# Kernel optimization log

Hardware: AMD Instinct MI355X
Metric: run time of the kernel (lower is better)

## Reference

```python
import jax, jax.numpy as jnp
import numpy as np

EPS_LN = 1e-5
EPS_NORM = 1e-12


def _bilinear_matrix(in_size, out_size):
    # align_corners=True bilinear interpolation as a dense (out,in) matrix
    pos = np.arange(out_size) * (in_size - 1) / (out_size - 1)
    lo = np.floor(pos).astype(np.int64)
    hi = np.minimum(lo + 1, in_size - 1)
    frac = (pos - lo).astype(np.float32)
    M = np.zeros((out_size, in_size), np.float32)
    M[np.arange(out_size), lo] += 1.0 - frac
    M[np.arange(out_size), hi] += frac
    return jnp.asarray(M)

_M20 = _bilinear_matrix(7, 20)  # [20,7]


def _upsample(x):
    # bilinear 7x7 -> 20x20, align_corners=True: separable matmuls
    return jnp.einsum('ih,jw,nchw->ncij', _M20, _M20, x)


def _conv2d(x, w, b, stride, pad):
    out = jax.lax.conv_general_dilated(
        x, w, window_strides=(stride, stride),
        padding=[(pad, pad), (pad, pad)],
        dimension_numbers=('NCHW', 'OIHW', 'NCHW'))
    return out + b[None, :, None, None]


def _crn(x, t, ln_w, ln_b, w_t, b_t, w_s, b_s, w_m, b_m, w_l, b_l, acc_w, acc_b):
    # LayerNorm over last two dims [7,7] with elementwise affine
    mu = x.mean(axis=(-2, -1), keepdims=True)
    var = x.var(axis=(-2, -1), keepdims=True)
    xn = (x - mu) * jax.lax.rsqrt(var + EPS_LN) * ln_w + ln_b
    up = _upsample(xn)                      # [N,512,20,20]
    xs = _conv2d(up, w_s, b_s, 3, 1)        # [N,32,7,7]
    xm = _conv2d(up, w_m, b_m, 5, 9)        # [N,32,7,7]
    xl = _conv2d(up, w_l, b_l, 2, 1)        # [N,20,7,7]
    tu = _upsample(t)
    tc = _conv2d(tu, w_t, b_t, 2, 0)        # [N,16,7,7]
    cat = jnp.concatenate([xs, xm, xl, tc], axis=1)  # [N,100,7,7]
    return _conv2d(cat, acc_w, acc_b, 1, 0)          # [N,1,7,7]


def setup_inputs() -> dict:
    key = jax.random.key(0)
    ks = jax.random.split(key, 16)
    N, C, K = 512, 512, 64
    centroids = jax.random.uniform(ks[0], (K, C), dtype=jnp.float32)
    return {
        'x': jax.random.normal(ks[1], (N, C, 7, 7), dtype=jnp.float32),
        't': jax.random.normal(ks[2], (N, C, 7, 7), dtype=jnp.float32),
        'centroids': centroids,
        'conv_w': 2.0 * 100.0 * centroids,
        'conv_b': -100.0 * jnp.linalg.norm(centroids, axis=1),
        'ln_w': jnp.ones((7, 7), jnp.float32),
        'ln_b': jnp.zeros((7, 7), jnp.float32),
        'w_t': jax.random.normal(ks[3], (16, 512, 8, 8), jnp.float32) * 0.02,
        'b_t': jax.random.normal(ks[4], (16,), jnp.float32) * 0.02,
        'w_s': jax.random.normal(ks[5], (32, 512, 3, 3), jnp.float32) * 0.02,
        'b_s': jax.random.normal(ks[6], (32,), jnp.float32) * 0.02,
        'w_m': jax.random.normal(ks[7], (32, 512, 7, 7), jnp.float32) * 0.02,
        'b_m': jax.random.normal(ks[8], (32,), jnp.float32) * 0.02,
        'w_l': jax.random.normal(ks[9], (20, 512, 9, 9), jnp.float32) * 0.02,
        'b_l': jax.random.normal(ks[10], (20,), jnp.float32) * 0.02,
        'acc_w': jax.random.normal(ks[11], (1, 100, 1, 1), jnp.float32) * 0.1,
        'acc_b': jax.random.normal(ks[12], (1,), jnp.float32) * 0.1,
    }


def reference(x, t, centroids, conv_w, conv_b, ln_w, ln_b,
              w_t, b_t, w_s, b_s, w_m, b_m, w_l, b_l, acc_w, acc_b):
    N, C = x.shape[:2]
    K = centroids.shape[0]
    S = x.shape[2] * x.shape[3]  # 49

    # CRN context weights [N,1,S]
    cw = _crn(x, t, ln_w, ln_b, w_t, b_t, w_s, b_s, w_m, b_m, w_l, b_l,
              acc_w, acc_b).reshape(N, 1, S)

    # descriptor-wise L2 normalization over channel dim (F.normalize p=2 dim=1)
    nrm = jnp.sqrt(jnp.sum(x * x, axis=1, keepdims=True))
    xn = x / jnp.maximum(nrm, EPS_NORM)
    xf = xn.reshape(N, C, S)                 # [N,C,S]

    # 1x1 conv == per-pixel matmul with conv_w [K,C]
    logits = jnp.einsum('kc,ncs->nks', conv_w, xf) + conv_b[None, :, None]
    sa = jax.nn.softmax(logits, axis=1)      # softmax over clusters

    w = sa * cw                              # reweighting mask [N,K,S]
    # matmul decomposition of sum_s w*(x - c): avoids (N,K,C,S) tensor
    vlad = (jnp.einsum('nks,ncs->nkc', w, xf)
            - centroids[None] * jnp.sum(w, axis=-1)[..., None])  # [N,K,C]

    # intra-normalize over C, flatten, global L2 normalize
    vn = jnp.sqrt(jnp.sum(vlad * vlad, axis=2, keepdims=True))
    vlad = vlad / jnp.maximum(vn, EPS_NORM)
    vlad = vlad.reshape(N, K * C)
    gn = jnp.sqrt(jnp.sum(vlad * vlad, axis=1, keepdims=True))
    return vlad / jnp.maximum(gn, EPS_NORM)
```

## Files before the change

### kernel.cpp

```cpp
#include <hip/hip_runtime.h>
#include <cstdint>
#include <cstddef>


#define N_   512
#define C_   512
#define S_   49
#define CS_  25088

#define OFF_WBS   0u
#define OFF_WBM   4608u
#define OFF_WBL   29696u
#define OFF_WBT   71168u
#define OFF_BETA  103936u
#define OFF_PLTH  136720u
#define OFF_PLTL  939536u
#define OFF_QTH   1742352u
#define OFF_QTL   2545168u
#define OFF_PWTH  3347984u
#define OFF_PWTL  3364368u
#define OFF_PB    3380752u
#define OFF_PBP   3380816u
#define OFF_MUR   3405904u
#define OFF_XS    3668048u
#define OFF_WR    3668048u
#define OFF_CWP2  16513104u
#define OFF_WSUM  19724368u
#define OFF_CENTT 19757136u
#define OFF_CWF   19789904u

typedef __attribute__((ext_vector_type(8))) short bf16x8;
typedef __attribute__((ext_vector_type(4))) float f32x4;

__device__ __forceinline__ float wave_sum64(float v) {
  #pragma unroll
  for (int off = 32; off; off >>= 1) v += __shfl_xor(v, off, 64);
  return v;
}

__device__ __forceinline__ void bsplit(float f, short& h, short& l) {
  unsigned u = __float_as_uint(f);
  h = (short)(u >> 16);
  float hf = __uint_as_float(u & 0xffff0000u);
  l = (short)(__float_as_uint(f - hf) >> 16);
}

__device__ __forceinline__ void bsplit3(float f, short& h, short& m, short& l) {
  unsigned u = __float_as_uint(f);
  h = (short)(u >> 16);
  float hf = __uint_as_float(u & 0xffff0000u);
  float r1 = f - hf;
  unsigned u1 = __float_as_uint(r1);
  m = (short)(u1 >> 16);
  float mf = __uint_as_float(u1 & 0xffff0000u);
  float r2 = r1 - mf;
  l = (short)(__float_as_uint(r2) >> 16);
}

__device__ __forceinline__ float m20val(int r, int p) {
  float pos = (float)(r * 6) / 19.0f;
  int lo = (int)floorf(pos);
  int hi = min(lo + 1, 6);
  float fr = pos - (float)lo;
  float v = 0.f;
  if (p == lo) v += 1.f - fr;
  if (p == hi) v += fr;
  return v;
}

__global__ void k_wbar(const float* __restrict__ w_s, const float* __restrict__ w_m,
                       const float* __restrict__ w_l, const float* __restrict__ w_t,
                       const float* __restrict__ accw, const float* __restrict__ accb,
                       const float* __restrict__ b_s, const float* __restrict__ b_m,
                       const float* __restrict__ b_l, const float* __restrict__ b_t,
                       float* __restrict__ wbs, float* __restrict__ wbm,
                       float* __restrict__ wbl, float* __restrict__ wbt,
                       float* __restrict__ beta) {
  int id = blockIdx.x * 256 + threadIdx.x;
  if (id == 0) {
    float b = accb[0];
    for (int o = 0; o < 32; ++o) b = fmaf(accw[o],      b_s[o], b);
    for (int o = 0; o < 32; ++o) b = fmaf(accw[32 + o], b_m[o], b);
    for (int o = 0; o < 20; ++o) b = fmaf(accw[64 + o], b_l[o], b);
    for (int o = 0; o < 16; ++o) b = fmaf(accw[84 + o], b_t[o], b);
    beta[0] = b;
  }
  if (id < 4608) {
    int c = id / 9, uv = id % 9;
    float a = 0.f;
    for (int o = 0; o < 32; ++o) a = fmaf(accw[o], w_s[(size_t)(o * 512 + c) * 9 + uv], a);
    wbs[id] = a;
  } else if (id < 29696) {
    int i2 = id - 4608; int c = i2 / 49, uv = i2 % 49;
    float a = 0.f;
    for (int o = 0; o < 32; ++o) a = fmaf(accw[32 + o], w_m[(size_t)(o * 512 + c) * 49 + uv], a);
    wbm[i2] = a;
  } else if (id < 71168) {
    int i2 = id - 29696; int c = i2 / 81, uv = i2 % 81;
    float a = 0.f;
    for (int o = 0; o < 20; ++o) a = fmaf(accw[64 + o], w_l[(size_t)(o * 512 + c) * 81 + uv], a);
    wbl[i2] = a;
  } else {
    int i2 = id - 71168; int c = i2 / 64, uv = i2 % 64;
    float a = 0.f;
    for (int o = 0; o < 16; ++o) a = fmaf(accw[84 + o], w_t[(size_t)(o * 512 + c) * 64 + uv], a);
    wbt[i2] = a;
  }
}

__global__ void k_wt(const float* __restrict__ convw, const float* __restrict__ cent,
                     short* __restrict__ cwfh, short* __restrict__ cwfm,
                     short* __restrict__ cwfl, float* __restrict__ centT) {
  int id = blockIdx.x * 256 + threadIdx.x;
  if (id < 32768) {
    int k = id >> 9, c = id & 511;
    short h, m, l; bsplit3(convw[(size_t)k * 512 + c], h, m, l);
    int kc = c >> 5, kg = (c >> 3) & 3, off = c & 7;
    int w = k >> 4, l15 = k & 15;
    int idx = ((kc * 4 + w) * 64 + kg * 16 + l15) * 8 + off;
    cwfh[idx] = h; cwfm[idx] = m; cwfl[idx] = l;
  } else {
    int id2 = id - 32768;
    int k = id2 & 63, c = id2 >> 6;
    centT[id2] = cent[(size_t)k * 512 + c];
  }
}

__global__ void k_xs(const float* __restrict__ x, float* __restrict__ xs,
                     float* __restrict__ mur) {
  int idx = blockIdx.x * 256 + threadIdx.x;
  const float* p = x + (size_t)idx * 49;
  float s1 = 0.f, s2 = 0.f;
  #pragma unroll
  for (int s = 0; s < 49; ++s) { float v = p[s]; s1 += v; s2 = fmaf(v, v, s2); }
  float m = s1 * (1.f / 49.f);
  float var = s2 * (1.f / 49.f) - m * m;
  float r = 1.f / sqrtf(var + 1e-5f);
  float* o = xs + (size_t)idx * 49;
  #pragma unroll
  for (int s = 0; s < 49; ++s) o[s] = p[s] * r;
  mur[idx] = m * r;
}

__global__ void __launch_bounds__(512) k_buildP(
    const float* __restrict__ wbs, const float* __restrict__ wbm,
    const float* __restrict__ wbl, const float* __restrict__ wbt,
    const float* __restrict__ lnw, const float* __restrict__ lnb,
    short* __restrict__ plth, short* __restrict__ pltl,
    short* __restrict__ qth,  short* __restrict__ qtl,
    short* __restrict__ pwth, short* __restrict__ pwtl,
    float* __restrict__ pbp) {
  __shared__ float M[20][7];
  __shared__ float tP[49][50];
  __shared__ float tQ[49][50];
  int c = blockIdx.x;
  int tid = threadIdx.x;
  if (tid < 140) { int r = tid / 7, p = tid % 7; M[r][p] = m20val(r, p); }
  __syncthreads();

  const float* wbsr = wbs + c * 9;
  const float* wbmr = wbm + c * 49;
  const float* wblr = wbl + c * 81;
  const float* wbtr = wbt + c * 64;

  for (int e = tid; e < 2401; e += 512) {
    int s = e / 49, q = e % 49;
    int i = q / 7, j = q % 7, pp = s / 7, qq = s % 7;

    float sumP = 0.f;
    {
      float rv[3];
      #pragma unroll
      for (int v = 0; v < 3; ++v) { int col = j * 3 - 1 + v; rv[v] = ((unsigned)col < 20u) ? M[col][qq] : 0.f; }
      #pragma unroll
      for (int u = 0; u < 3; ++u) {
        int row = i * 3 - 1 + u; float ru = ((unsigned)row < 20u) ? M[row][pp] : 0.f;
        float a = wbsr[u * 3 + 0] * rv[0];
        a = fmaf(wbsr[u * 3 + 1], rv[1], a);
        a = fmaf(wbsr[u * 3 + 2], rv[2], a);
        sumP = fmaf(ru, a, sumP);
      }
    }
    {
      float rv[7];
      #pragma unroll
      for (int v = 0; v < 7; ++v) { int col = j * 5 - 9 + v; rv[v] = ((unsigned)col < 20u) ? M[col][qq] : 0.f; }
      #pragma unroll
      for (int u = 0; u < 7; ++u) {
        int row = i * 5 - 9 + u; float ru = ((unsigned)row < 20u) ? M[row][pp] : 0.f;
        float a = 0.f;
        #pragma unroll
        for (int v = 0; v < 7; ++v) a = fmaf(wbmr[u * 7 + v], rv[v], a);
        sumP = fmaf(ru, a, sumP);
      }
    }
    {
      float rv[9];
      #pragma unroll
      for (int v = 0; v < 9; ++v) { int col = j * 2 - 1 + v; rv[v] = ((unsigned)col < 20u) ? M[col][qq] : 0.f; }
      #pragma unroll
      for (int u = 0; u < 9; ++u) {
        int row = i * 2 - 1 + u; float ru = ((unsigned)row < 20u) ? M[row][pp] : 0.f;
        float a = 0.f;
        #pragma unroll
        for (int v = 0; v < 9; ++v) a = fmaf(wblr[u * 9 + v], rv[v], a);
        sumP = fmaf(ru, a, sumP);
      }
    }
    tP[s][q] = sumP;

    float sumQ = 0.f;
    {
      float rv[8];
      #pragma unroll
      for (int v = 0; v < 8; ++v) { int col = j * 2 + v; rv[v] = ((unsigned)col < 20u) ? M[col][qq] : 0.f; }
      #pragma unroll
      for (int u = 0; u < 8; ++u) {
        int row = i * 2 + u; float ru = ((unsigned)row < 20u) ? M[row][pp] : 0.f;
        float a = 0.f;
        #pragma unroll
        for (int v = 0; v < 8; ++v) a = fmaf(wbtr[u * 8 + v], rv[v], a);
        sumQ = fmaf(ru, a, sumQ);
      }
    }
    tQ[s][q] = sumQ;
  }
  __syncthreads();

  for (int e = tid; e < 2401; e += 512) {
    int q = e / 49, s = e % 49;
    float pv = tP[s][q];
    float qv = tQ[s][q];
    int k = c * 49 + s;
    int slab = k >> 8;
    int kc = (k & 255) >> 5;
    int kg = (k >> 3) & 3;
    int off = k & 7;
    int nf = q >> 4, l15 = q & 15;
    size_t oidx = (size_t)slab * 16384 + kc * 2048 + nf * 512
                + (size_t)(kg * 16 + l15) * 8 + off;
    short h, l;
    bsplit(lnw[s] * pv, h, l); plth[oidx] = h; pltl[oidx] = l;
    bsplit(qv, h, l);          qth[oidx]  = h; qtl[oidx]  = l;
  }

  if (tid < 49) {
    int q = tid;
    float pw = 0.f, pb = 0.f;
    #pragma unroll 7
    for (int s = 0; s < 49; ++s) {
      float p = tP[s][q];
      pw = fmaf(lnw[s], p, pw);
      pb = fmaf(lnb[s], p, pb);
    }
    short h, l; bsplit(-pw, h, l);
    pwth[q * 512 + c] = h;
    pwtl[q * 512 + c] = l;
    pbp[q * 512 + c] = pb;
  }
}

__global__ void k_pb(const float* __restrict__ pbp, float* __restrict__ PB) {
  int q = blockIdx.x, lane = threadIdx.x;
  float a = 0.f;
  for (int c = lane; c < 512; c += 64) a += pbp[q * 512 + c];
  a = wave_sum64(a);
  if (lane == 0) PB[q] = a;
}

template <int SA, int SB>
__device__ __forceinline__ void mf_chunk1(const float* __restrict__ A,
                                          const short* __restrict__ Bh,
                                          const short* __restrict__ Bl,
                                          int k, int mbase, int l15, int kg,
                                          f32x4 (&acc)[4]) {
  bf16x8 ah, al;
  {
    const float* ap = A + (size_t)(mbase + l15) * SA + k + kg * 8;
    float4 v0 = *reinterpret_cast<const float4*>(ap);
    float4 v1 = *reinterpret_cast<const float4*>(ap + 4);
    float f[8] = {v0.x, v0.y, v0.z, v0.w, v1.x, v1.y, v1.z, v1.w};
    #pragma unroll
    for (int jj = 0; jj < 8; ++jj) { short hh, ll; bsplit(f[jj], hh, ll); ah[jj] = hh; al[jj] = ll; }
  }
  #pragma unroll
  for (int nf = 0; nf < 4; ++nf) {
    size_t bo = (size_t)(nf * 16 + l15) * SB + k + kg * 8;
    bf16x8 bh = *reinterpret_cast<const bf16x8*>(Bh + bo);
    bf16x8 bl = *reinterpret_cast<const bf16x8*>(Bl + bo);
    acc[nf] = __builtin_amdgcn_mfma_f32_16x16x32_bf16(ah, bh, acc[nf], 0, 0, 0);
    acc[nf] = __builtin_amdgcn_mfma_f32_16x16x32_bf16(ah, bl, acc[nf], 0, 0, 0);
    acc[nf] = __builtin_amdgcn_mfma_f32_16x16x32_bf16(al, bh, acc[nf], 0, 0, 0);
  }
}

__global__ void __launch_bounds__(64) k_cwg(
    const float* __restrict__ xs, const float* __restrict__ tin,
    const float* __restrict__ mur,
    const short* __restrict__ plth, const short* __restrict__ pltl,
    const short* __restrict__ qth,  const short* __restrict__ qtl,
    const short* __restrict__ pwth, const short* __restrict__ pwtl,
    float* __restrict__ cwp2) {
  __shared__ float at[16 * 272];
  int wgid = (blockIdx.x & 7) * 392 + (blockIdx.x >> 3);
  int slab = wgid >> 5, mt = wgid & 31;
  int lane = threadIdx.x;
  int l15 = lane & 15, kg = lane >> 4;
  int mbase = mt * 16;
  int k0 = slab * 256;

  f32x4 acc[4];
  #pragma unroll
  for (int nf = 0; nf < 4; ++nf) acc[nf] = (f32x4){0.f, 0.f, 0.f, 0.f};

  #pragma unroll 1
  for (int ph = 0; ph < 2; ++ph) {
    const float* A  = ph ? tin : xs;
    const short* Bh = ph ? qth : plth;
    const short* Bl = ph ? qtl : pltl;
    const short* bhb = Bh + (size_t)slab * 16384 + lane * 8;
    const short* blb = Bl + (size_t)slab * 16384 + lane * 8;

    bf16x8 pbh[2][4], pbl[2][4];
    #pragma unroll
    for (int nf = 0; nf < 4; ++nf) {
      pbh[0][nf] = *reinterpret_cast<const bf16x8*>(bhb + nf * 512);
      pbl[0][nf] = *reinterpret_cast<const bf16x8*>(blb + nf * 512);
    }

    __syncthreads();
    #pragma unroll
    for (int i = 0; i < 16; ++i) {
      int idx4 = i * 64 + lane;
      int row = idx4 >> 6, col4 = idx4 & 63;
      float4 v = *reinterpret_cast<const float4*>(
          &A[(size_t)(mbase + row) * CS_ + k0 + col4 * 4]);
      *reinterpret_cast<float4*>(&at[row * 272 + col4 * 4]) = v;
    }
    __syncthreads();

    #pragma unroll
    for (int kc = 0; kc < 8; ++kc) {
      int cur = kc & 1, nxt = cur ^ 1;
      if (kc < 7) {
        #pragma unroll
        for (int nf = 0; nf < 4; ++nf) {
          pbh[nxt][nf] = *reinterpret_cast<const bf16x8*>(bhb + (kc + 1) * 2048 + nf * 512);
          pbl[nxt][nf] = *reinterpret_cast<const bf16x8*>(blb + (kc + 1) * 2048 + nf * 512);
        }
      }
      bf16x8 ah, al;
      {
        const float* ap = &at[l15 * 272 + kc * 32 + kg * 8];
        float4 v0 = *reinterpret_cast<const float4*>(ap);
        float4 v1 = *reinterpret_cast<const float4*>(ap + 4);
        float f[8] = {v0.x, v0.y, v0.z, v0.w, v1.x, v1.y, v1.z, v1.w};
        #pragma unroll
        for (int jj = 0; jj < 8; ++jj) { short hh, ll; bsplit(f[jj], hh, ll); ah[jj] = hh; al[jj] = ll; }
      }
      #pragma unroll
      for (int nf = 0; nf < 4; ++nf) {
        acc[nf] = __builtin_amdgcn_mfma_f32_16x16x32_bf16(ah, pbh[cur][nf], acc[nf], 0, 0, 0);
        acc[nf] = __builtin_amdgcn_mfma_f32_16x16x32_bf16(ah, pbl[cur][nf], acc[nf], 0, 0, 0);
        acc[nf] = __builtin_amdgcn_mfma_f32_16x16x32_bf16(al, pbh[cur][nf], acc[nf], 0, 0, 0);
      }
    }
  }
  if (slab < 16)
    mf_chunk1<512, 512>(mur, pwth, pwtl, slab * 32, mbase, l15, kg, acc);

  #pragma unroll
  for (int nf = 0; nf < 4; ++nf)
    #pragma unroll
    for (int r = 0; r < 4; ++r) {
      int row = mbase + kg * 4 + r;
      int col = nf * 16 + l15;
      cwp2[(size_t)slab * 32768 + (size_t)row * 64 + col] = acc[nf][r];
    }
}

__global__ void __launch_bounds__(256) k_logits(
    const float* __restrict__ x,
    const short* __restrict__ cwfh, const short* __restrict__ cwfm,
    const short* __restrict__ cwfl,
    const float* __restrict__ convb, const float* __restrict__ cwp2,
    const float* __restrict__ beta, const float* __restrict__ pb,
    float* __restrict__ wr, float* __restrict__ wsum) {
  __shared__ float sh[64 * 140];
  __shared__ float sqp[4][49];
  __shared__ float cw4[4 * 49];
  __shared__ float mx4[4 * 49];
  __shared__ float sm4[4 * 49];
  float* xt = sh;
  float* part2 = sh;
  int n = blockIdx.x;
  int tid = threadIdx.x;
  int w = tid >> 6, lane = tid & 63;
  int l15 = lane & 15, kg = lane >> 4;
  float* pf = part2;
  const float* xb = x + (size_t)n * CS_;

  for (int e = tid; e < 960; e += 256) {
    int kq = e / 15, p = e % 15;
    wr[((size_t)n * 64 + kq) * 64 + 49 + p] = 0.f;
  }
  for (int e = tid; e < 1920; e += 256) {
    int row = 49 + e / 128, col = e % 128;
    xt[row * 140 + col] = 0.f;
  }

  if (tid < 196) {
    int s = tid % 49, g = tid / 49;
    int st = (g < 2) ? g * 25 : 50 + (g - 2) * 24;
    int cnt = (g < 2) ? 25 : 24;
    const float* cp = cwp2 + (size_t)st * 32768 + (size_t)n * 64 + s;
    float a = 0.f;
    for (int i = 0; i < cnt; ++i) a += cp[(size_t)i * 32768];
    cw4[g * 49 + s] = a;
  }

  int scol = tid % 49, sgrp = tid / 49;
  float ssql = 0.f;
  f32x4 acc[4];
  #pragma unroll
  for (int nf = 0; nf < 4; ++nf) acc[nf] = (f32x4){0.f, 0.f, 0.f, 0.f};

  #pragma unroll 1
  for (int h = 0; h < 4; ++h) {
    int c0 = h * 128;
    __syncthreads();
    for (int e = tid; e < 6272; e += 256) {
      int c_row = e / 49, col = e % 49;
      xt[col * 140 + c_row] = xb[(size_t)c0 * 49 + e];
    }
    __syncthreads();

    if (tid < 196) {
      #pragma unroll 8
      for (int j = 0; j < 32; ++j) {
        float v = xt[scol * 140 + sgrp * 32 + j];
        ssql = fmaf(v, v, ssql);
      }
    }

    #pragma unroll
    for (int kcl = 0; kcl < 4; ++kcl) {
      int kc = h * 4 + kcl;
      bf16x8 ah = *reinterpret_cast<const bf16x8*>(cwfh + ((kc * 4 + w) * 64 + lane) * 8);
      bf16x8 am = *reinterpret_cast<const bf16x8*>(cwfm + ((kc * 4 + w) * 64 + lane) * 8);
      bf16x8 al = *reinterpret_cast<const bf16x8*>(cwfl + ((kc * 4 + w) * 64 + lane) * 8);
      #pragma unroll
      for (int nf = 0; nf < 4; ++nf) {
        const float* bp = &xt[(nf * 16 + l15) * 140 + kcl * 32 + kg * 8];
        float4 v0 = *reinterpret_cast<const float4*>(bp);
        float4 v1 = *reinterpret_cast<const float4*>(bp + 4);
        float f[8] = {v0.x, v0.y, v0.z, v0.w, v1.x, v1.y, v1.z, v1.w};
        bf16x8 bh, bm, bl;
        #pragma unroll
        for (int jj = 0; jj < 8; ++jj) {
          short hh, mm, ll; bsplit3(f[jj], hh, mm, ll);
          bh[jj] = hh; bm[jj] = mm; bl[jj] = ll;
        }
        acc[nf] = __builtin_amdgcn_mfma_f32_16x16x32_bf16(ah, bh, acc[nf], 0, 0, 0);
        acc[nf] = __builtin_amdgcn_mfma_f32_16x16x32_bf16(ah, bm, acc[nf], 0, 0, 0);
        acc[nf] = __builtin_amdgcn_mfma_f32_16x16x32_bf16(am, bh, acc[nf], 0, 0, 0);
        acc[nf] = __builtin_amdgcn_mfma_f32_16x16x32_bf16(ah, bl, acc[nf], 0, 0, 0);
        acc[nf] = __builtin_amdgcn_mfma_f32_16x16x32_bf16(am, bm, acc[nf], 0, 0, 0);
        acc[nf] = __builtin_amdgcn_mfma_f32_16x16x32_bf16(al, bh, acc[nf], 0, 0, 0);
      }
    }
  }
  __syncthreads();

  #pragma unroll
  for (int nf = 0; nf < 4; ++nf)
    #pragma unroll
    for (int r = 0; r < 4; ++r) {
      int s = nf * 16 + l15;
      if (s < 49) part2[(w * 16 + kg * 4 + r) * 52 + s] = acc[nf][r];
    }
  if (tid < 196) sqp[sgrp][scol] = ssql;
  __syncthreads();

  float lg[16];
  int sg = tid / 49, s_ = tid % 49;
  float rnv = 0.f;
  if (tid < 196) {
    float sumsq = sqp[0][s_] + sqp[1][s_] + sqp[2][s_] + sqp[3][s_];
    rnv = 1.f / fmaxf(sqrtf(sumsq), 1e-12f);
    float mloc = -1e30f;
    #pragma unroll
    for (int kk = 0; kk < 16; ++kk) {
      int kq = sg * 16 + kk;
      lg[kk] = fmaf(part2[kq * 52 + s_], rnv, convb[kq]);
      mloc = fmaxf(mloc, lg[kk]);
    }
    mx4[sg * 49 + s_] = mloc;
  }
  __syncthreads();
  if (tid < 196) {
    float m0 = fmaxf(fmaxf(mx4[s_], mx4[49 + s_]), fmaxf(mx4[98 + s_], mx4[147 + s_]));
    float sloc = 0.f;
    #pragma unroll
    for (int kk = 0; kk < 16; ++kk) { lg[kk] = expf(lg[kk] - m0); sloc += lg[kk]; }
    sm4[sg * 49 + s_] = sloc;
  }
  __syncthreads();
  if (tid < 196) {
    float ssum = sm4[s_] + sm4[49 + s_] + sm4[98 + s_] + sm4[147 + s_];
    float cwv = cw4[s_] + cw4[49 + s_] + cw4[98 + s_] + cw4[147 + s_] + beta[0] + pb[s_];
    float inv = cwv / ssum;
    float wrs = inv * rnv;
    #pragma unroll
    for (int kk = 0; kk < 16; ++kk) {
      int kq = sg * 16 + kk;
      wr[((size_t)n * 64 + kq) * 64 + s_] = lg[kk] * wrs;
      pf[kq * 49 + s_] = lg[kk] * inv;
    }
  }
  __syncthreads();
  if (tid < 64) {
    float a = 0.f;
    #pragma unroll 7
    for (int s = 0; s < 49; ++s) a += pf[tid * 49 + s];
    wsum[n * 64 + tid] = a;
  }
}

__global__ void __launch_bounds__(256) k_vlad(
    const float* __restrict__ x, const float* __restrict__ wr,
    const float* __restrict__ wsum, const float* __restrict__ centT,
    float* __restrict__ out) {
  __shared__ float sh[128 * 68];
  __shared__ float sp[16][64];
  __shared__ float scal[64];
  float* xt = sh;
  float* vl = sh;
  int n = blockIdx.x;
  int tid = threadIdx.x;
  int w = tid >> 6, lane = tid & 63;
  int l15 = lane & 15, kg = lane >> 4;
  const float* xb = x + (size_t)n * CS_;
  const float* wrb = wr + (size_t)n * 4096;
  const float* wsb = wsum + n * 64;
  float* ob = out + (size_t)n * 32768;

  float wsk[4];
  #pragma unroll
  for (int nf = 0; nf < 4; ++nf) wsk[nf] = wsb[nf * 16 + l15];
  float ssqa[4] = {0.f, 0.f, 0.f, 0.f};

  #pragma unroll 1
  for (int h = 0; h < 4; ++h) {
    int c0 = h * 128;
    __syncthreads();
    for (int e = tid; e < 6272; e += 256) {
      int row = e / 49, col = e % 49;
      xt[row * 68 + col] = xb[(size_t)c0 * 49 + e];
    }
    for (int e = tid; e < 1920; e += 256) {
      int row = e / 15, col = 49 + e % 15;
      xt[row * 68 + col] = 0.f;
    }
    __syncthreads();

    f32x4 acc[2][4];
    #pragma unroll
    for (int mf = 0; mf < 2; ++mf)
      #pragma unroll
      for (int nf = 0; nf < 4; ++nf)
        acc[mf][nf] = (f32x4){0.f, 0.f, 0.f, 0.f};

    #pragma unroll
    for (int kc = 0; kc < 2; ++kc) {
      bf16x8 bh[4], bl[4];
      #pragma unroll
      for (int nf = 0; nf < 4; ++nf) {
        const float* bp = wrb + (nf * 16 + l15) * 64 + kc * 32 + kg * 8;
        float4 v0 = *reinterpret_cast<const float4*>(bp);
        float4 v1 = *reinterpret_cast<const float4*>(bp + 4);
        float f[8] = {v0.x, v0.y, v0.z, v0.w, v1.x, v1.y, v1.z, v1.w};
        #pragma unroll
        for (int jj = 0; jj < 8; ++jj) { short hh, ll; bsplit(f[jj], hh, ll); bh[nf][jj] = hh; bl[nf][jj] = ll; }
      }
      #pragma unroll
      for (int mf = 0; mf < 2; ++mf) {
        bf16x8 ah, al;
        {
          const float* ap = &xt[(w * 32 + mf * 16 + l15) * 68 + kc * 32 + kg * 8];
          float4 v0 = *reinterpret_cast<const float4*>(ap);
          float4 v1 = *reinterpret_cast<const float4*>(ap + 4);
          float f[8] = {v0.x, v0.y, v0.z, v0.w, v1.x, v1.y, v1.z, v1.w};
          #pragma unroll
          for (int jj = 0; jj < 8; ++jj) { short hh, ll; bsplit(f[jj], hh, ll); ah[jj] = hh; al[jj] = ll; }
        }
        #pragma unroll
        for (int nf = 0; nf < 4; ++nf) {
          acc[mf][nf] = __builtin_amdgcn_mfma_f32_16x16x32_bf16(ah, bh[nf], acc[mf][nf], 0, 0, 0);
          acc[mf][nf] = __builtin_amdgcn_mfma_f32_16x16x32_bf16(ah, bl[nf], acc[mf][nf], 0, 0, 0);
          acc[mf][nf] = __builtin_amdgcn_mfma_f32_16x16x32_bf16(al, bh[nf], acc[mf][nf], 0, 0, 0);
        }
      }
    }
    __syncthreads();

    #pragma unroll
    for (int mf = 0; mf < 2; ++mf)
      #pragma unroll
      for (int nf = 0; nf < 4; ++nf)
        #pragma unroll
        for (int r = 0; r < 4; ++r) {
          int cc = w * 32 + mf * 16 + kg * 4 + r;
          int c = c0 + cc;
          int k = nf * 16 + l15;
          float v = fmaf(-centT[c * 64 + k], wsk[nf], acc[mf][nf][r]);
          vl[k * 129 + cc] = v;
          ssqa[nf] = fmaf(v, v, ssqa[nf]);
        }
    __syncthreads();
    #pragma unroll 4
    for (int e = tid; e < 8192; e += 256) {
      int k = e >> 7, cc = e & 127;
      ob[(size_t)k * 512 + c0 + cc] = vl[k * 129 + cc];
    }
  }

  #pragma unroll
  for (int nf = 0; nf < 4; ++nf) sp[w * 4 + kg][nf * 16 + l15] = ssqa[nf];
  __syncthreads();
  if (tid < 64) {
    float v2 = 0.f;
    #pragma unroll
    for (int j = 0; j < 16; ++j) v2 += sp[j][tid];
    float vn = sqrtf(v2);
    float den = fmaxf(vn, 1e-12f);
    float cr = vn / den; cr *= cr;
    float g = wave_sum64(cr);
    scal[tid] = 1.f / (den * fmaxf(sqrtf(g), 1e-12f));
  }
  __syncthreads();
  #pragma unroll 8
  for (int idx = tid; idx < 32768; idx += 256)
    ob[idx] *= scal[idx >> 9];
}

extern "C" void kernel_launch(void* const* d_in, const int* in_sizes, int n_in,
                              void* d_out, int out_size, void* d_ws, size_t ws_size,
                              hipStream_t stream) {
  const float* x     = (const float*)d_in[0];
  const float* t     = (const float*)d_in[1];
  const float* cent  = (const float*)d_in[2];
  const float* convw = (const float*)d_in[3];
  const float* convb = (const float*)d_in[4];
  const float* lnw   = (const float*)d_in[5];
  const float* lnb   = (const float*)d_in[6];
  const float* w_t   = (const float*)d_in[7];
  const float* b_t   = (const float*)d_in[8];
  const float* w_s   = (const float*)d_in[9];
  const float* b_s   = (const float*)d_in[10];
  const float* w_m   = (const float*)d_in[11];
  const float* b_m   = (const float*)d_in[12];
  const float* w_l   = (const float*)d_in[13];
  const float* b_l   = (const float*)d_in[14];
  const float* accw  = (const float*)d_in[15];
  const float* accb  = (const float*)d_in[16];
  float* ws  = (float*)d_ws;
  float* out = (float*)d_out;

  float* wbs  = ws + OFF_WBS;
  float* wbm  = ws + OFF_WBM;
  float* wbl  = ws + OFF_WBL;
  float* wbt  = ws + OFF_WBT;
  float* beta = ws + OFF_BETA;
  short* cwfh = (short*)(ws + OFF_CWF);
  short* cwfm = (short*)(ws + OFF_CWF + 16384);
  short* cwfl = (short*)(ws + OFF_CWF + 32768);
  short* plth = (short*)(ws + OFF_PLTH);
  short* pltl = (short*)(ws + OFF_PLTL);
  short* qth  = (short*)(ws + OFF_QTH);
  short* qtl  = (short*)(ws + OFF_QTL);
  short* pwth = (short*)(ws + OFF_PWTH);
  short* pwtl = (short*)(ws + OFF_PWTL);
  float* PB   = ws + OFF_PB;
  float* pbp  = ws + OFF_PBP;
  float* mur  = ws + OFF_MUR;
  float* xs   = ws + OFF_XS;
  float* cwp2 = ws + OFF_CWP2;
  float* wr   = ws + OFF_WR;
  float* wsumb = ws + OFF_WSUM;
  float* centT = ws + OFF_CENTT;

  k_wbar<<<dim3(406), dim3(256), 0, stream>>>(w_s, w_m, w_l, w_t, accw, accb,
                                              b_s, b_m, b_l, b_t,
                                              wbs, wbm, wbl, wbt, beta);
  k_wt<<<dim3(256), dim3(256), 0, stream>>>(convw, cent, cwfh, cwfm, cwfl, centT);
  k_xs<<<dim3(1024), dim3(256), 0, stream>>>(x, xs, mur);
  hipMemsetAsync(ws + OFF_PLTH, 0, (size_t)3244032 * 4, stream);
  k_buildP<<<dim3(512), dim3(512), 0, stream>>>(wbs, wbm, wbl, wbt, lnw, lnb,
                                                plth, pltl, qth, qtl,
                                                pwth, pwtl, pbp);
  k_pb<<<dim3(49), dim3(64), 0, stream>>>(pbp, PB);
  k_cwg<<<dim3(3136), dim3(64), 0, stream>>>(xs, t, mur, plth, pltl, qth, qtl,
                                             pwth, pwtl, cwp2);
  k_logits<<<dim3(512), dim3(256), 0, stream>>>(x, cwfh, cwfm, cwfl, convb, cwp2,
                                                beta, PB, wr, wsumb);
  k_vlad<<<dim3(512), dim3(256), 0, stream>>>(x, wr, wsumb, centT, out);
}
```

Measured before the change: 223.0 us.

## Split VLAD into norm pass and recompute-and-scale output pass

The fused VLAD kernel wrote the unnormalized output, then re-read and rescaled it in place. It is now two kernels: the first computes per-cluster sums of squares over half the channels per block, and the second recomputes the matmul and writes the already-scaled result once. This removes the read-modify-write pass over the large output and doubles the grid to 1024 blocks for more parallelism. In exchange the x·wr matmul and the reads of x are done twice, and there is one more launch.

Result: no change. 219.9 us (-1.4%).

```diff
diff --git a/kernel.cpp b/kernel.cpp
--- a/kernel.cpp
+++ b/kernel.cpp
@@ -28,6 +28,7 @@
 #define OFF_WSUM  19724368u
 #define OFF_CENTT 19757136u
 #define OFF_CWF   19789904u
+#define OFF_SSQ2  19839056u
 
 typedef __attribute__((ext_vector_type(8))) short bf16x8;
 typedef __attribute__((ext_vector_type(4))) float f32x4;
@@ -527,23 +528,24 @@
   }
 }
 
-__global__ void __launch_bounds__(256) k_vlad(
+__global__ void __launch_bounds__(256) k_vssq(
     const float* __restrict__ x, const float* __restrict__ wr,
     const float* __restrict__ wsum, const float* __restrict__ centT,
-    float* __restrict__ out) {
-  __shared__ float sh[128 * 68];
+    float* __restrict__ ssqp2) {
+  __shared__ float xt[128 * 68];
   __shared__ float sp[16][64];
-  __shared__ float scal[64];
-  float* xt = sh;
-  float* vl = sh;
-  int n = blockIdx.x;
+  int n = blockIdx.x >> 1, ch = blockIdx.x & 1;
   int tid = threadIdx.x;
   int w = tid >> 6, lane = tid & 63;
   int l15 = lane & 15, kg = lane >> 4;
   const float* xb = x + (size_t)n * CS_;
   const float* wrb = wr + (size_t)n * 4096;
   const float* wsb = wsum + n * 64;
-  float* ob = out + (size_t)n * 32768;
+
+  for (int e = tid; e < 1920; e += 256) {
+    int row = e / 15, col = 49 + e % 15;
+    xt[row * 68 + col] = 0.f;
+  }
 
   float wsk[4];
   #pragma unroll
@@ -551,16 +553,12 @@
   float ssqa[4] = {0.f, 0.f, 0.f, 0.f};
 
   #pragma unroll 1
-  for (int h = 0; h < 4; ++h) {
-    int c0 = h * 128;
+  for (int hh = 0; hh < 2; ++hh) {
+    int c0 = (ch * 2 + hh) * 128;
     __syncthreads();
     for (int e = tid; e < 6272; e += 256) {
       int row = e / 49, col = e % 49;
       xt[row * 68 + col] = xb[(size_t)c0 * 49 + e];
-    }
-    for (int e = tid; e < 1920; e += 256) {
-      int row = e / 15, col = 49 + e % 15;
-      xt[row * 68 + col] = 0.f;
     }
     __syncthreads();
 
@@ -581,7 +579,7 @@
         float4 v1 = *reinterpret_cast<const float4*>(bp + 4);
         float f[8] = {v0.x, v0.y, v0.z, v0.w, v1.x, v1.y, v1.z, v1.w};
         #pragma unroll
-        for (int jj = 0; jj < 8; ++jj) { short hh, ll; bsplit(f[jj], hh, ll); bh[nf][jj] = hh; bl[nf][jj] = ll; }
+        for (int jj = 0; jj < 8; ++jj) { short hh2, ll; bsplit(f[jj], hh2, ll); bh[nf][jj] = hh2; bl[nf][jj] = ll; }
       }
       #pragma unroll
       for (int mf = 0; mf < 2; ++mf) {
@@ -592,7 +590,7 @@
           float4 v1 = *reinterpret_cast<const float4*>(ap + 4);
           float f[8] = {v0.x, v0.y, v0.z, v0.w, v1.x, v1.y, v1.z, v1.w};
           #pragma unroll
-          for (int jj = 0; jj < 8; ++jj) { short hh, ll; bsplit(f[jj], hh, ll); ah[jj] = hh; al[jj] = ll; }
+          for (int jj = 0; jj < 8; ++jj) { short hh2, ll; bsplit(f[jj], hh2, ll); ah[jj] = hh2; al[jj] = ll; }
         }
         #pragma unroll
         for (int nf = 0; nf < 4; ++nf) {
@@ -602,7 +600,6 @@
         }
       }
     }
-    __syncthreads();
 
     #pragma unroll
     for (int mf = 0; mf < 2; ++mf)
@@ -614,15 +611,8 @@
           int c = c0 + cc;
           int k = nf * 16 + l15;
           float v = fmaf(-centT[c * 64 + k], wsk[nf], acc[mf][nf][r]);
-          vl[k * 129 + cc] = v;
           ssqa[nf] = fmaf(v, v, ssqa[nf]);
         }
-    __syncthreads();
-    #pragma unroll 4
-    for (int e = tid; e < 8192; e += 256) {
-      int k = e >> 7, cc = e & 127;
-      ob[(size_t)k * 512 + c0 + cc] = vl[k * 129 + cc];
-    }
   }
 
   #pragma unroll
@@ -632,16 +622,113 @@
     float v2 = 0.f;
     #pragma unroll
     for (int j = 0; j < 16; ++j) v2 += sp[j][tid];
+    ssqp2[(size_t)(n * 2 + ch) * 64 + tid] = v2;
+  }
+}
+
+__global__ void __launch_bounds__(256) k_vout(
+    const float* __restrict__ x, const float* __restrict__ wr,
+    const float* __restrict__ wsum, const float* __restrict__ centT,
+    const float* __restrict__ ssqp2, float* __restrict__ out) {
+  __shared__ float sh[128 * 68];
+  __shared__ float scal[64];
+  float* xt = sh;
+  float* vl = sh;
+  int n = blockIdx.x >> 1, ch = blockIdx.x & 1;
+  int tid = threadIdx.x;
+  int w = tid >> 6, lane = tid & 63;
+  int l15 = lane & 15, kg = lane >> 4;
+  const float* xb = x + (size_t)n * CS_;
+  const float* wrb = wr + (size_t)n * 4096;
+  const float* wsb = wsum + n * 64;
+  float* ob = out + (size_t)n * 32768;
+
+  if (tid < 64) {
+    float v2 = ssqp2[(size_t)n * 128 + tid] + ssqp2[(size_t)n * 128 + 64 + tid];
     float vn = sqrtf(v2);
     float den = fmaxf(vn, 1e-12f);
     float cr = vn / den; cr *= cr;
     float g = wave_sum64(cr);
     scal[tid] = 1.f / (den * fmaxf(sqrtf(g), 1e-12f));
   }
-  __syncthreads();
-  #pragma unroll 8
-  for (int idx = tid; idx < 32768; idx += 256)
-    ob[idx] *= scal[idx >> 9];
+
+  float wsk[4];
+  #pragma unroll
+  for (int nf = 0; nf < 4; ++nf) wsk[nf] = wsb[nf * 16 + l15];
+
+  #pragma unroll 1
+  for (int hh = 0; hh < 2; ++hh) {
+    int c0 = (ch * 2 + hh) * 128;
+    __syncthreads();
+    for (int e = tid; e < 6272; e += 256) {
+      int row = e / 49, col = e % 49;
+      xt[row * 68 + col] = xb[(size_t)c0 * 49 + e];
+    }
+    for (int e = tid; e < 1920; e += 256) {
+      int row = e / 15, col = 49 + e % 15;
+      xt[row * 68 + col] = 0.f;
+    }
+    __syncthreads();
+
+    f32x4 acc[2][4];
+    #pragma unroll
+    for (int mf = 0; mf < 2; ++mf)
+      #pragma unroll
+      for (int nf = 0; nf < 4; ++nf)
+        acc[mf][nf] = (f32x4){0.f, 0.f, 0.f, 0.f};
+
+    #pragma unroll
+    for (int kc = 0; kc < 2; ++kc) {
+      bf16x8 bh[4], bl[4];
+      #pragma unroll
+      for (int nf = 0; nf < 4; ++nf) {
+        const float* bp = wrb + (nf * 16 + l15) * 64 + kc * 32 + kg * 8;
+        float4 v0 = *reinterpret_cast<const float4*>(bp);
+        float4 v1 = *reinterpret_cast<const float4*>(bp + 4);
+        float f[8] = {v0.x, v0.y, v0.z, v0.w, v1.x, v1.y, v1.z, v1.w};
+        #pragma unroll
+        for (int jj = 0; jj < 8; ++jj) { short hh2, ll; bsplit(f[jj], hh2, ll); bh[nf][jj] = hh2; bl[nf][jj] = ll; }
+      }
+      #pragma unroll
+      for (int mf = 0; mf < 2; ++mf) {
+        bf16x8 ah, al;
+        {
+          const float* ap = &xt[(w * 32 + mf * 16 + l15) * 68 + kc * 32 + kg * 8];
+          float4 v0 = *reinterpret_cast<const float4*>(ap);
+          float4 v1 = *reinterpret_cast<const float4*>(ap + 4);
+          float f[8] = {v0.x, v0.y, v0.z, v0.w, v1.x, v1.y, v1.z, v1.w};
+          #pragma unroll
+          for (int jj = 0; jj < 8; ++jj) { short hh2, ll; bsplit(f[jj], hh2, ll); ah[jj] = hh2; al[jj] = ll; }
+        }
+        #pragma unroll
+        for (int nf = 0; nf < 4; ++nf) {
+          acc[mf][nf] = __builtin_amdgcn_mfma_f32_16x16x32_bf16(ah, bh[nf], acc[mf][nf], 0, 0, 0);
+          acc[mf][nf] = __builtin_amdgcn_mfma_f32_16x16x32_bf16(ah, bl[nf], acc[mf][nf], 0, 0, 0);
+          acc[mf][nf] = __builtin_amdgcn_mfma_f32_16x16x32_bf16(al, bh[nf], acc[mf][nf], 0, 0, 0);
+        }
+      }
+    }
+    __syncthreads();
+
+    #pragma unroll
+    for (int mf = 0; mf < 2; ++mf)
+      #pragma unroll
+      for (int nf = 0; nf < 4; ++nf)
+        #pragma unroll
+        for (int r = 0; r < 4; ++r) {
+          int cc = w * 32 + mf * 16 + kg * 4 + r;
+          int c = c0 + cc;
+          int k = nf * 16 + l15;
+          float v = fmaf(-centT[c * 64 + k], wsk[nf], acc[mf][nf][r]);
+          vl[k * 129 + cc] = v * scal[k];
+        }
+    __syncthreads();
+    #pragma unroll 4
+    for (int e = tid; e < 8192; e += 256) {
+      int k = e >> 7, cc = e & 127;
+      ob[(size_t)k * 512 + c0 + cc] = vl[k * 129 + cc];
+    }
+  }
 }
 
 extern "C" void kernel_launch(void* const* d_in, const int* in_sizes, int n_in,
@@ -689,6 +776,7 @@
   float* wr   = ws + OFF_WR;
   float* wsumb = ws + OFF_WSUM;
   float* centT = ws + OFF_CENTT;
+  float* ssqp2 = ws + OFF_SSQ2;
 
   k_wbar<<<dim3(406), dim3(256), 0, stream>>>(w_s, w_m, w_l, w_t, accw, accb,
                                               b_s, b_m, b_l, b_t,
@@ -704,5 +792,6 @@
                                              pwth, pwtl, cwp2);
   k_logits<<<dim3(512), dim3(256), 0, stream>>>(x, cwfh, cwfm, cwfl, convb, cwp2,
                                                 beta, PB, wr, wsumb);
-  k_vlad<<<dim3(512), dim3(256), 0, stream>>>(x, wr, wsumb, centT, out);
-}
+  k_vssq<<<dim3(1024), dim3(256), 0, stream>>>(x, wr, wsumb, centT, ssqp2);
+  k_vout<<<dim3(1024), dim3(256), 0, stream>>>(x, wr, wsumb, centT, ssqp2, out);
+}
```
